# Kernel tuning notes

Hardware: AMD Instinct MI355X
Metric: run time of the kernel (lower is better)

## Reference

```python
import jax, jax.numpy as jnp
import numpy as np

EPS = 1e-07
DEGREE = 3
INPUT_DIM = 256
OUTPUT_DIM = 256
BATCH = 2048


def setup_inputs() -> dict:
    key = jax.random.key(0)
    kx, kc = jax.random.split(key)
    x = jax.random.normal(kx, (BATCH, INPUT_DIM), dtype=jnp.float32)
    std = 1.0 / (INPUT_DIM * (DEGREE + 1))
    cheby_coeffs = jax.random.normal(kc, (INPUT_DIM, OUTPUT_DIM, DEGREE + 1), dtype=jnp.float32) * std
    return {"x": x, "cheby_coeffs": cheby_coeffs}


def reference(x, cheby_coeffs):
    # x: [b, i]; cheby_coeffs: [i, o, d+1]
    input_dim = x.shape[1]
    degree_p1 = cheby_coeffs.shape[2]
    arange = jnp.arange(degree_p1, dtype=x.dtype)  # [d+1]
    t = jnp.tanh(x)
    theta = jnp.arccos(jnp.clip(t, -1.0 + EPS, 1.0 - EPS))  # [b, i]
    basis = jnp.cos(theta[:, :, None] * arange)  # [b, i, d+1] Chebyshev T_k
    # Fused contraction: einsum 'bid,iod->bio' followed by sum over i == 'bid,iod->bo'
    y = jnp.einsum('bid,iod->bo', basis, cheby_coeffs) / input_dim
    return y
```

## Files before the change

kernel.cpp:

```cpp
#include <hip/hip_runtime.h>
#include <stdint.h>

#define I_DIM   256
#define O_DIM   256
#define BM      32
#define BN      32
#define NCH     4

typedef float f32x4 __attribute__((ext_vector_type(4)));
typedef short bf16x8 __attribute__((ext_vector_type(8)));

__device__ __forceinline__ uint32_t f2bf(float f) {
    uint32_t u = __builtin_bit_cast(uint32_t, f);
    u += 0x7fffu + ((u >> 16) & 1u);
    return u >> 16;
}

__device__ __forceinline__ float fast_tanh(float v) {
    float e = __expf(2.0f * v);
    return 1.0f - 2.0f / (e + 1.0f);
}

__device__ __forceinline__ void basis_words(float v, uint32_t& lo, uint32_t& hi) {
    const float CLIP = 0.99999994f;
    float t = fast_tanh(v);
    t = fminf(CLIP, fmaxf(-CLIP, t));
    float t2 = __builtin_fmaf(2.0f * t, t, -1.0f);
    float t3 = __builtin_fmaf(2.0f * t, t2, -t);
    lo = 0x3f80u | (f2bf(t) << 16);
    hi = f2bf(t2) | (f2bf(t3) << 16);
}

__global__ __launch_bounds__(256, 2) void cheby_mfma(
        const float* __restrict__ x, const float* __restrict__ cc,
        float* __restrict__ out) {
    __shared__ __align__(16) unsigned char lds[65536];

    const int tid  = threadIdx.x;
    const int lane = tid & 63;
    const int wid  = tid >> 6;
    const int bm   = blockIdx.x >> 3;
    const int bn   = blockIdx.x & 7;
    const int m0   = bm * BM;
    const int n0   = bn * BN;

    const int arow = tid >> 3;
    const int aiq  = tid & 7;
    const int bcl  = tid & 31;
    const int big  = tid >> 5;

    const float4* __restrict__ x4 = reinterpret_cast<const float4*>(x);
    const float4* __restrict__ c4 = reinterpret_cast<const float4*>(cc);

    float4 ax0, ax1;
    float4 cb[8];

    auto loadAB = [&](int ch) {
        const float4* p = &x4[(m0 + arow) * (I_DIM / 4) + ch * 16 + aiq * 2];
        ax0 = p[0]; ax1 = p[1];
        #pragma unroll
        for (int j = 0; j < 8; ++j)
            cb[j] = c4[(ch * 64 + big * 8 + j) * O_DIM + n0 + bcl];
    };

    auto stageAB = [&](int d) {
        const uint32_t abase = (uint32_t)(d * 16384 + arow * 512 + aiq * 64);
        const uint32_t axr   = (uint32_t)((arow & 31) << 4);
        uint32_t w0, w1, w2, w3, w4, w5, w6, w7;
        basis_words(ax0.x, w0, w1); basis_words(ax0.y, w2, w3);
        basis_words(ax0.z, w4, w5); basis_words(ax0.w, w6, w7);
        *reinterpret_cast<uint4*>(lds + ((abase     ) ^ axr)) = make_uint4(w0, w1, w2, w3);
        *reinterpret_cast<uint4*>(lds + ((abase + 16) ^ axr)) = make_uint4(w4, w5, w6, w7);
        basis_words(ax1.x, w0, w1); basis_words(ax1.y, w2, w3);
        basis_words(ax1.z, w4, w5); basis_words(ax1.w, w6, w7);
        *reinterpret_cast<uint4*>(lds + ((abase + 32) ^ axr)) = make_uint4(w0, w1, w2, w3);
        *reinterpret_cast<uint4*>(lds + ((abase + 48) ^ axr)) = make_uint4(w4, w5, w6, w7);
        const uint32_t bbase = (uint32_t)(32768 + d * 16384 + bcl * 512 + big * 64);
        const uint32_t bxr   = (uint32_t)((bcl & 31) << 4);
        #pragma unroll
        for (int j = 0; j < 8; j += 2) {
            uint32_t u0 = f2bf(cb[j].x)     | (f2bf(cb[j].y) << 16);
            uint32_t u1 = f2bf(cb[j].z)     | (f2bf(cb[j].w) << 16);
            uint32_t u2 = f2bf(cb[j + 1].x) | (f2bf(cb[j + 1].y) << 16);
            uint32_t u3 = f2bf(cb[j + 1].z) | (f2bf(cb[j + 1].w) << 16);
            *reinterpret_cast<uint4*>(lds + ((bbase + j * 8) ^ bxr)) = make_uint4(u0, u1, u2, u3);
        }
    };

    const int wr = wid >> 1, wc = wid & 1;
    const int mrow  = wr * 16 + (lane & 15);
    const int bcol  = wc * 16 + (lane & 15);
    const int klane = (lane >> 4) << 3;
    const uint32_t aswz = (uint32_t)((mrow & 31) << 4);
    const uint32_t bswz = (uint32_t)((bcol & 31) << 4);

    f32x4 acc0 = {0.f, 0.f, 0.f, 0.f};
    f32x4 acc1 = {0.f, 0.f, 0.f, 0.f};

    loadAB(0);
    #pragma unroll
    for (int ch = 0; ch < NCH; ++ch) {
        stageAB(ch & 1);
        if (ch + 1 < NCH) loadAB(ch + 1);
        __syncthreads();
        const uint32_t abase = (uint32_t)((ch & 1) * 16384 + mrow * 512);
        const uint32_t bbase = (uint32_t)(32768 + (ch & 1) * 16384 + bcol * 512);
        #pragma unroll
        for (int ks = 0; ks < 8; ++ks) {
            const uint32_t kb = (uint32_t)((ks * 32 + klane) * 2);
            bf16x8 a = *reinterpret_cast<const bf16x8*>(lds + ((abase + kb) ^ aswz));
            bf16x8 b = *reinterpret_cast<const bf16x8*>(lds + ((bbase + kb) ^ bswz));
            if (ks & 1) acc1 = __builtin_amdgcn_mfma_f32_16x16x32_bf16(a, b, acc1, 0, 0, 0);
            else        acc0 = __builtin_amdgcn_mfma_f32_16x16x32_bf16(a, b, acc0, 0, 0, 0);
        }
        if (ch + 1 < NCH) __syncthreads();
    }

    const float sc = 1.0f / 256.0f;
    f32x4 r = (acc0 + acc1);
    const int gr = m0 + wr * 16 + ((lane >> 4) << 2);
    const int gc = n0 + wc * 16 + (lane & 15);
    #pragma unroll
    for (int q = 0; q < 4; ++q)
        out[(gr + q) * O_DIM + gc] = r[q] * sc;
}

extern "C" void kernel_launch(void* const* d_in, const int* in_sizes, int n_in,
                              void* d_out, int out_size, void* d_ws, size_t ws_size,
                              hipStream_t stream) {
    (void)in_sizes; (void)n_in; (void)out_size; (void)d_ws; (void)ws_size;
    const float* x  = (const float*)d_in[0];
    const float* cc = (const float*)d_in[1];
    float* out = (float*)d_out;
    cheby_mfma<<<dim3(512), dim3(256), 0, stream>>>(x, cc, out);
}
```

Before: 14.41 us.

## Split into basis/bf16 prep kernel plus direct-from-global MFMA GEMM

Adds a prep kernel that computes the Chebyshev basis of x once and converts the coefficients to transposed bf16 in workspace, then a GEMM kernel that streams MFMA operands straight from global memory with no LDS or barriers. This removes the repeated per-tile basis and conversion work (each x row was recomputed for 8 column tiles) and the LDS staging. The cost is a second launch and a round trip of about 5 MB through workspace. The fused kernel is kept as a fallback when the workspace is too small.

```diff
diff --git a/kernel.cpp b/kernel.cpp
--- a/kernel.cpp
+++ b/kernel.cpp
@@ -3,9 +3,8 @@
 
 #define I_DIM   256
 #define O_DIM   256
-#define BM      32
-#define BN      32
-#define NCH     4
+#define B_ROWS  2048
+#define KK      1024
 
 typedef float f32x4 __attribute__((ext_vector_type(4)));
 typedef short bf16x8 __attribute__((ext_vector_type(8)));
@@ -31,11 +30,79 @@
     hi = f2bf(t2) | (f2bf(t3) << 16);
 }
 
-__global__ __launch_bounds__(256, 2) void cheby_mfma(
+__global__ __launch_bounds__(256) void cheby_prep(
+        const float* __restrict__ x, const float* __restrict__ cc,
+        uint16_t* __restrict__ A, uint16_t* __restrict__ Bt) {
+    const int task = blockIdx.x * 256 + threadIdx.x;
+    if (task < 262144) {
+        const int row = task >> 7;
+        const int h   = task & 127;
+        float2 v = reinterpret_cast<const float2*>(x)[row * 128 + h];
+        uint32_t l0, h0, l1, h1;
+        basis_words(v.x, l0, h0);
+        basis_words(v.y, l1, h1);
+        *reinterpret_cast<uint4*>(reinterpret_cast<char*>(A) + row * 2048 + h * 16) =
+            make_uint4(l0, h0, l1, h1);
+    } else {
+        const int t = task - 262144;
+        const int i = t >> 8;
+        const int o = t & 255;
+        float4 c = reinterpret_cast<const float4*>(cc)[i * 256 + o];
+        uint32_t u0 = f2bf(c.x) | (f2bf(c.y) << 16);
+        uint32_t u1 = f2bf(c.z) | (f2bf(c.w) << 16);
+        *reinterpret_cast<uint2*>(reinterpret_cast<char*>(Bt) + o * 2048 + i * 8) =
+            make_uint2(u0, u1);
+    }
+}
+
+__global__ __launch_bounds__(256, 2) void cheby_gemm(
+        const uint16_t* __restrict__ A, const uint16_t* __restrict__ Bt,
+        float* __restrict__ out) {
+    const int tid  = threadIdx.x;
+    const int lane = tid & 63;
+    const int wid  = tid >> 6;
+    const int m    = blockIdx.x & 63;
+    const int bn   = blockIdx.x >> 6;
+    const int m0   = m * 32;
+    const int n0   = bn * 32;
+    const int wr   = wid >> 1, wc = wid & 1;
+
+    const int arow = m0 + wr * 16 + (lane & 15);
+    const int bcol = n0 + wc * 16 + (lane & 15);
+    const int koff = (lane >> 4) << 3;
+
+    const uint16_t* ap = A  + arow * KK + koff;
+    const uint16_t* bp = Bt + bcol * KK + koff;
+
+    f32x4 acc0 = {0.f, 0.f, 0.f, 0.f};
+    f32x4 acc1 = {0.f, 0.f, 0.f, 0.f};
+
+    #pragma unroll
+    for (int ks = 0; ks < 32; ks += 2) {
+        bf16x8 a0 = *reinterpret_cast<const bf16x8*>(ap + ks * 32);
+        bf16x8 b0 = *reinterpret_cast<const bf16x8*>(bp + ks * 32);
+        bf16x8 a1 = *reinterpret_cast<const bf16x8*>(ap + ks * 32 + 32);
+        bf16x8 b1 = *reinterpret_cast<const bf16x8*>(bp + ks * 32 + 32);
+        acc0 = __builtin_amdgcn_mfma_f32_16x16x32_bf16(a0, b0, acc0, 0, 0, 0);
+        acc1 = __builtin_amdgcn_mfma_f32_16x16x32_bf16(a1, b1, acc1, 0, 0, 0);
+    }
+
+    const float sc = 1.0f / 256.0f;
+    f32x4 r = acc0 + acc1;
+    const int gr = m0 + wr * 16 + ((lane >> 4) << 2);
+    const int gc = n0 + wc * 16 + (lane & 15);
+    #pragma unroll
+    for (int q = 0; q < 4; ++q)
+        out[(gr + q) * O_DIM + gc] = r[q] * sc;
+}
+
+#define BM 32
+#define BN 32
+#define NCH 4
+__global__ __launch_bounds__(256, 2) void cheby_fused(
         const float* __restrict__ x, const float* __restrict__ cc,
         float* __restrict__ out) {
     __shared__ __align__(16) unsigned char lds[65536];
-
     const int tid  = threadIdx.x;
     const int lane = tid & 63;
     const int wid  = tid >> 6;
@@ -43,26 +110,17 @@
     const int bn   = blockIdx.x & 7;
     const int m0   = bm * BM;
     const int n0   = bn * BN;
-
-    const int arow = tid >> 3;
-    const int aiq  = tid & 7;
-    const int bcl  = tid & 31;
-    const int big  = tid >> 5;
-
-    const float4* __restrict__ x4 = reinterpret_cast<const float4*>(x);
-    const float4* __restrict__ c4 = reinterpret_cast<const float4*>(cc);
-
-    float4 ax0, ax1;
-    float4 cb[8];
-
+    const int arow = tid >> 3, aiq = tid & 7;
+    const int bcl  = tid & 31, big = tid >> 5;
+    const float4* x4 = reinterpret_cast<const float4*>(x);
+    const float4* c4 = reinterpret_cast<const float4*>(cc);
+    float4 ax0, ax1, cb[8];
     auto loadAB = [&](int ch) {
         const float4* p = &x4[(m0 + arow) * (I_DIM / 4) + ch * 16 + aiq * 2];
         ax0 = p[0]; ax1 = p[1];
         #pragma unroll
-        for (int j = 0; j < 8; ++j)
-            cb[j] = c4[(ch * 64 + big * 8 + j) * O_DIM + n0 + bcl];
+        for (int j = 0; j < 8; ++j) cb[j] = c4[(ch * 64 + big * 8 + j) * O_DIM + n0 + bcl];
     };
-
     auto stageAB = [&](int d) {
         const uint32_t abase = (uint32_t)(d * 16384 + arow * 512 + aiq * 64);
         const uint32_t axr   = (uint32_t)((arow & 31) << 4);
@@ -86,17 +144,13 @@
             *reinterpret_cast<uint4*>(lds + ((bbase + j * 8) ^ bxr)) = make_uint4(u0, u1, u2, u3);
         }
     };
-
     const int wr = wid >> 1, wc = wid & 1;
-    const int mrow  = wr * 16 + (lane & 15);
-    const int bcol  = wc * 16 + (lane & 15);
+    const int mrow = wr * 16 + (lane & 15);
+    const int bcol = wc * 16 + (lane & 15);
     const int klane = (lane >> 4) << 3;
     const uint32_t aswz = (uint32_t)((mrow & 31) << 4);
     const uint32_t bswz = (uint32_t)((bcol & 31) << 4);
-
-    f32x4 acc0 = {0.f, 0.f, 0.f, 0.f};
-    f32x4 acc1 = {0.f, 0.f, 0.f, 0.f};
-
+    f32x4 acc0 = {0.f,0.f,0.f,0.f}, acc1 = {0.f,0.f,0.f,0.f};
     loadAB(0);
     #pragma unroll
     for (int ch = 0; ch < NCH; ++ch) {
@@ -115,22 +169,29 @@
         }
         if (ch + 1 < NCH) __syncthreads();
     }
-
     const float sc = 1.0f / 256.0f;
-    f32x4 r = (acc0 + acc1);
+    f32x4 r = acc0 + acc1;
     const int gr = m0 + wr * 16 + ((lane >> 4) << 2);
     const int gc = n0 + wc * 16 + (lane & 15);
     #pragma unroll
-    for (int q = 0; q < 4; ++q)
-        out[(gr + q) * O_DIM + gc] = r[q] * sc;
+    for (int q = 0; q < 4; ++q) out[(gr + q) * O_DIM + gc] = r[q] * sc;
 }
 
 extern "C" void kernel_launch(void* const* d_in, const int* in_sizes, int n_in,
                               void* d_out, int out_size, void* d_ws, size_t ws_size,
                               hipStream_t stream) {
-    (void)in_sizes; (void)n_in; (void)out_size; (void)d_ws; (void)ws_size;
+    (void)in_sizes; (void)n_in; (void)out_size;
     const float* x  = (const float*)d_in[0];
     const float* cc = (const float*)d_in[1];
     float* out = (float*)d_out;
-    cheby_mfma<<<dim3(512), dim3(256), 0, stream>>>(x, cc, out);
+    const size_t needA  = (size_t)B_ROWS * KK * 2;
+    const size_t needBt = (size_t)O_DIM * KK * 2;
+    if (ws_size >= needA + needBt) {
+        uint16_t* Abuf  = (uint16_t*)d_ws;
+        uint16_t* Btbuf = (uint16_t*)((char*)d_ws + needA);
+        cheby_prep<<<dim3(1280), dim3(256), 0, stream>>>(x, cc, Abuf, Btbuf);
+        cheby_gemm<<<dim3(512), dim3(256), 0, stream>>>(Abuf, Btbuf, out);
+    } else {
+        cheby_fused<<<dim3(512), dim3(256), 0, stream>>>(x, cc, out);
+    }
 }
```

Measured after the change: 26.16 us. +81.5%, slower.
